# Kernel tuning notes

Measured on AMD Instinct MI355X. Metric: run time of the kernel, lower is better.

The kernel has to match this reference:

```python
import jax, jax.numpy as jnp
import numpy as np

NUM_TYPES = 4  # unique atom types, e.g. H,C,N,O
N_DESC = 384   # descriptor width (nDescriptors())


def setup_inputs() -> dict:
    key = jax.random.key(0)
    k1, k2, k3 = jax.random.split(key, 3)
    n_confs, n_atoms = 2048, 64
    coords = jax.random.normal(k1, (n_confs, n_atoms, 3), dtype=jnp.float32)
    atom_types = jax.random.randint(k2, (n_confs, n_atoms), 0, NUM_TYPES, dtype=jnp.int64)
    W = jax.random.normal(k3, (3, N_DESC), dtype=jnp.float32)
    return {"coords": coords, "atom_types": atom_types, "W": W}


def reference(coords, atom_types, W):
    n_confs, n_atoms, _ = coords.shape
    # stub descriptor computer: per-atom descriptor, (n_confs*n_atoms, N_DESC)
    desc = jnp.tanh(coords.reshape(-1, 3) @ W)
    at2type = atom_types.reshape(-1)                      # (N,)
    # conformer index for every atom: [0,0,...,0,1,1,...]
    at2conf = jnp.repeat(jnp.arange(n_confs, dtype=jnp.int64), n_atoms)
    # stable sort by atom type (routing permutation)
    perm = jnp.argsort(at2type, stable=True)              # (N,)
    desc_sorted = desc[perm]                              # gather (N, N_DESC)
    at2conf_sorted = at2conf[perm]                        # (N,)
    at_type_count = jnp.bincount(at2type, length=NUM_TYPES)  # split sizes per type
    # per-type buckets = desc_sorted split at cumsum(at_type_count); returned
    # concatenated with counts to keep shapes static under jit.
    return desc_sorted, at2conf_sorted, at_type_count
```

## Files before the change

kernel.cpp:

```cpp
#include <hip/hip_runtime.h>

#define NDESC 384
#define NTYPES 4
#define ATOMS_PER_CONF 64
#define BLOCK_ATOMS 128

typedef unsigned int uint32;
typedef unsigned long long u64;

__device__ __forceinline__ float fast_tanh(float x) {
  float e = __builtin_amdgcn_exp2f(x * 2.8853900817779268f);
  return 1.0f - 2.0f * __builtin_amdgcn_rcpf(1.0f + e);
}

__global__ __launch_bounds__(BLOCK_ATOMS) void hist_kernel(
    const int* __restrict__ types, uint32* __restrict__ blockHist, int n) {
  __shared__ uint32 cnt[NTYPES];
  int tid = threadIdx.x;
  if (tid < NTYPES) cnt[tid] = 0;
  __syncthreads();
  int idx = blockIdx.x * BLOCK_ATOMS + tid;
  int ty = (idx < n) ? types[idx] : -1;
  int lane = tid & 63;
  for (int t = 0; t < NTYPES; ++t) {
    u64 m = __ballot(ty == t);
    if (lane == 0) atomicAdd(&cnt[t], (uint32)__popcll(m));
  }
  __syncthreads();
  if (tid < NTYPES) blockHist[blockIdx.x * NTYPES + tid] = cnt[tid];
}

__global__ __launch_bounds__(256) void scan_kernel(
    const uint32* __restrict__ blockHist, uint32* __restrict__ blockOff,
    float* __restrict__ outCounts, int nb) {
  __shared__ uint32 totals[NTYPES];
  int tid = threadIdx.x;
  int wave = tid >> 6;
  int lane = tid & 63;

  uint32 sum = 0;
  for (int b = lane; b < nb; b += 64) sum += blockHist[b * NTYPES + wave];
  for (int off = 32; off > 0; off >>= 1) sum += __shfl_down(sum, off);
  if (lane == 0) totals[wave] = sum;
  __syncthreads();

  uint32 base = 0;
  for (int t = 0; t < wave; ++t) base += totals[t];

  uint32 carry = 0;
  for (int c = 0; c * 64 < nb; ++c) {
    int b = c * 64 + lane;
    uint32 v = (b < nb) ? blockHist[b * NTYPES + wave] : 0;
    uint32 orig = v;
    for (int off = 1; off < 64; off <<= 1) {
      uint32 nv = __shfl_up(v, off);
      if (lane >= off) v += nv;
    }
    if (b < nb) blockOff[b * NTYPES + wave] = base + carry + (v - orig);
    carry += __shfl(v, 63);
  }
  if (tid < NTYPES) outCounts[tid] = (float)totals[tid];
}

__global__ __launch_bounds__(384) void main_kernel(
    const float* __restrict__ coords, const int* __restrict__ types,
    const float* __restrict__ W, const uint32* __restrict__ blockOff,
    float* __restrict__ descOut, float* __restrict__ confOut, int n) {
  __shared__ float sW[3 * NDESC];
  __shared__ float sC[BLOCK_ATOMS][3];
  __shared__ uint32 sPos[BLOCK_ATOMS];
  __shared__ int sValid[BLOCK_ATOMS];
  __shared__ uint32 waveCnt[BLOCK_ATOMS / 64][NTYPES];

  int tid = threadIdx.x;
  int base = blockIdx.x * BLOCK_ATOMS;

  for (int i = tid; i < 3 * NDESC; i += 384) sW[i] = W[i];
  if (tid < BLOCK_ATOMS * 3) {
    int g = base * 3 + tid;
    sC[tid / 3][tid % 3] = (g < n * 3) ? coords[g] : 0.0f;
  }

  int idx = base + tid;
  int ty = -1;
  if (tid < BLOCK_ATOMS && idx < n) ty = types[idx];
  int wave = tid >> 6, lane = tid & 63;
  int myrank = 0;
  if (tid < BLOCK_ATOMS) {
    for (int t = 0; t < NTYPES; ++t) {
      u64 m = __ballot(ty == t);
      if (lane == 0) waveCnt[wave][t] = (uint32)__popcll(m);
      if (t == ty) myrank = (int)__popcll(m & ((1ull << lane) - 1ull));
    }
  }
  __syncthreads();
  if (tid < BLOCK_ATOMS) {
    if (ty >= 0) {
      for (int w = 0; w < wave; ++w) myrank += (int)waveCnt[w][ty];
      uint32 pos = blockOff[blockIdx.x * NTYPES + ty] + (uint32)myrank;
      sPos[tid] = pos;
      sValid[tid] = 1;
      confOut[pos] = (float)(idx >> 6);
    } else {
      sPos[tid] = 0;
      sValid[tid] = 0;
    }
  }
  __syncthreads();

  int r = tid / 96;
  int c = tid - r * 96;
  int d0 = 4 * c;
  float w00 = sW[d0], w01 = sW[d0 + 1], w02 = sW[d0 + 2], w03 = sW[d0 + 3];
  float w10 = sW[NDESC + d0], w11 = sW[NDESC + d0 + 1],
        w12 = sW[NDESC + d0 + 2], w13 = sW[NDESC + d0 + 3];
  float w20 = sW[2 * NDESC + d0], w21 = sW[2 * NDESC + d0 + 1],
        w22 = sW[2 * NDESC + d0 + 2], w23 = sW[2 * NDESC + d0 + 3];

  bool full = (base + BLOCK_ATOMS <= n);
  if (full) {
#pragma unroll 4
    for (int a0 = 0; a0 < BLOCK_ATOMS; a0 += 4) {
      int a = a0 + r;
      uint32 pos = sPos[a];
      float c0 = sC[a][0], c1 = sC[a][1], c2 = sC[a][2];
      float4 v;
      v.x = fast_tanh(c0 * w00 + c1 * w10 + c2 * w20);
      v.y = fast_tanh(c0 * w01 + c1 * w11 + c2 * w21);
      v.z = fast_tanh(c0 * w02 + c1 * w12 + c2 * w22);
      v.w = fast_tanh(c0 * w03 + c1 * w13 + c2 * w23);
      *reinterpret_cast<float4*>(descOut + pos * (uint32)NDESC + d0) = v;
    }
  } else {
    for (int a0 = 0; a0 < BLOCK_ATOMS; a0 += 4) {
      int a = a0 + r;
      uint32 pos = sPos[a];
      float c0 = sC[a][0], c1 = sC[a][1], c2 = sC[a][2];
      float4 v;
      v.x = fast_tanh(c0 * w00 + c1 * w10 + c2 * w20);
      v.y = fast_tanh(c0 * w01 + c1 * w11 + c2 * w21);
      v.z = fast_tanh(c0 * w02 + c1 * w12 + c2 * w22);
      v.w = fast_tanh(c0 * w03 + c1 * w13 + c2 * w23);
      if (sValid[a]) {
        *reinterpret_cast<float4*>(descOut + pos * (uint32)NDESC + d0) = v;
      }
    }
  }
}

extern "C" void kernel_launch(void* const* d_in, const int* in_sizes, int n_in,
                              void* d_out, int out_size, void* d_ws, size_t ws_size,
                              hipStream_t stream) {
  const float* coords = (const float*)d_in[0];
  const int* types = (const int*)d_in[1];
  const float* W = (const float*)d_in[2];

  int n = in_sizes[1];
  int nb = (n + BLOCK_ATOMS - 1) / BLOCK_ATOMS;

  uint32* blockHist = (uint32*)d_ws;
  uint32* blockOff = blockHist + (size_t)nb * NTYPES;

  float* descOut = (float*)d_out;
  float* confOut = descOut + (size_t)n * NDESC;
  float* countsOut = confOut + n;

  hipLaunchKernelGGL(hist_kernel, dim3(nb), dim3(BLOCK_ATOMS), 0, stream,
                     types, blockHist, n);
  hipLaunchKernelGGL(scan_kernel, dim3(1), dim3(256), 0, stream,
                     blockHist, blockOff, countsOut, nb);
  hipLaunchKernelGGL(main_kernel, dim3(nb), dim3(384), 0, stream,
                     coords, types, W, blockOff, descOut, confOut, n);
}
```

Measured before the change: 53.03 us.

## Fuse histogram, scan and scatter into one cooperative kernel with grid sync

Replaces the three-kernel pipeline (per-block type histogram, single-block scan, scatter/compute) with one cooperative kernel. Each block publishes its type histogram, waits at a grid-wide barrier, then computes its own prefix offsets and per-type totals by reducing the histogram array directly. Block size doubles to 256 atoms so the grid is small enough to be co-resident. This removes two kernel launches and the serial single-block scan. In exchange, every block has to be resident at once, and the barrier stalls all blocks until the slowest has finished its histogram.

```diff
diff --git a/kernel.cpp b/kernel.cpp
--- a/kernel.cpp
+++ b/kernel.cpp
@@ -1,84 +1,42 @@
 #include <hip/hip_runtime.h>
+#include <hip/hip_cooperative_groups.h>
 
 #define NDESC 384
 #define NTYPES 4
-#define ATOMS_PER_CONF 64
-#define BLOCK_ATOMS 128
+#define BLOCK_ATOMS 256
+#define NTHREADS 384
 
 typedef unsigned int uint32;
 typedef unsigned long long u64;
+
+namespace cg = cooperative_groups;
 
 __device__ __forceinline__ float fast_tanh(float x) {
   float e = __builtin_amdgcn_exp2f(x * 2.8853900817779268f);
   return 1.0f - 2.0f * __builtin_amdgcn_rcpf(1.0f + e);
 }
 
-__global__ __launch_bounds__(BLOCK_ATOMS) void hist_kernel(
-    const int* __restrict__ types, uint32* __restrict__ blockHist, int n) {
-  __shared__ uint32 cnt[NTYPES];
-  int tid = threadIdx.x;
-  if (tid < NTYPES) cnt[tid] = 0;
-  __syncthreads();
-  int idx = blockIdx.x * BLOCK_ATOMS + tid;
-  int ty = (idx < n) ? types[idx] : -1;
-  int lane = tid & 63;
-  for (int t = 0; t < NTYPES; ++t) {
-    u64 m = __ballot(ty == t);
-    if (lane == 0) atomicAdd(&cnt[t], (uint32)__popcll(m));
-  }
-  __syncthreads();
-  if (tid < NTYPES) blockHist[blockIdx.x * NTYPES + tid] = cnt[tid];
-}
-
-__global__ __launch_bounds__(256) void scan_kernel(
-    const uint32* __restrict__ blockHist, uint32* __restrict__ blockOff,
-    float* __restrict__ outCounts, int nb) {
-  __shared__ uint32 totals[NTYPES];
-  int tid = threadIdx.x;
-  int wave = tid >> 6;
-  int lane = tid & 63;
-
-  uint32 sum = 0;
-  for (int b = lane; b < nb; b += 64) sum += blockHist[b * NTYPES + wave];
-  for (int off = 32; off > 0; off >>= 1) sum += __shfl_down(sum, off);
-  if (lane == 0) totals[wave] = sum;
-  __syncthreads();
-
-  uint32 base = 0;
-  for (int t = 0; t < wave; ++t) base += totals[t];
-
-  uint32 carry = 0;
-  for (int c = 0; c * 64 < nb; ++c) {
-    int b = c * 64 + lane;
-    uint32 v = (b < nb) ? blockHist[b * NTYPES + wave] : 0;
-    uint32 orig = v;
-    for (int off = 1; off < 64; off <<= 1) {
-      uint32 nv = __shfl_up(v, off);
-      if (lane >= off) v += nv;
-    }
-    if (b < nb) blockOff[b * NTYPES + wave] = base + carry + (v - orig);
-    carry += __shfl(v, 63);
-  }
-  if (tid < NTYPES) outCounts[tid] = (float)totals[tid];
-}
-
-__global__ __launch_bounds__(384) void main_kernel(
+__global__ __launch_bounds__(NTHREADS, 3) void fused_kernel(
     const float* __restrict__ coords, const int* __restrict__ types,
-    const float* __restrict__ W, const uint32* __restrict__ blockOff,
-    float* __restrict__ descOut, float* __restrict__ confOut, int n) {
+    const float* __restrict__ W, uint32* __restrict__ blockHist,
+    float* __restrict__ descOut, float* __restrict__ confOut,
+    float* __restrict__ countsOut, int n, int nb) {
   __shared__ float sW[3 * NDESC];
   __shared__ float sC[BLOCK_ATOMS][3];
   __shared__ uint32 sPos[BLOCK_ATOMS];
   __shared__ int sValid[BLOCK_ATOMS];
   __shared__ uint32 waveCnt[BLOCK_ATOMS / 64][NTYPES];
+  __shared__ uint32 sTot[NTYPES];
+  __shared__ uint32 sOff[NTYPES];
 
   int tid = threadIdx.x;
-  int base = blockIdx.x * BLOCK_ATOMS;
+  int bid = blockIdx.x;
+  int base = bid * BLOCK_ATOMS;
 
-  for (int i = tid; i < 3 * NDESC; i += 384) sW[i] = W[i];
-  if (tid < BLOCK_ATOMS * 3) {
-    int g = base * 3 + tid;
-    sC[tid / 3][tid % 3] = (g < n * 3) ? coords[g] : 0.0f;
+  for (int i = tid; i < 3 * NDESC; i += NTHREADS) sW[i] = W[i];
+  for (int i = tid; i < BLOCK_ATOMS * 3; i += NTHREADS) {
+    int g = base * 3 + i;
+    sC[i / 3][i % 3] = (g < n * 3) ? coords[g] : 0.0f;
   }
 
   int idx = base + tid;
@@ -94,10 +52,43 @@
     }
   }
   __syncthreads();
+  if (tid < NTYPES) {
+    uint32 s = 0;
+    for (int w = 0; w < BLOCK_ATOMS / 64; ++w) s += waveCnt[w][tid];
+    blockHist[bid * NTYPES + tid] = s;
+  }
+  if (tid < BLOCK_ATOMS && ty >= 0) {
+    for (int w = 0; w < wave; ++w) myrank += (int)waveCnt[w][ty];
+  }
+
+  cg::this_grid().sync();
+
+  if (wave < NTYPES) {
+    int t = wave;
+    uint32 tot = 0, pre = 0;
+    for (int b = lane; b < nb; b += 64) {
+      uint32 h = blockHist[b * NTYPES + t];
+      tot += h;
+      if (b < bid) pre += h;
+    }
+    for (int off = 32; off > 0; off >>= 1) {
+      tot += __shfl_down(tot, off);
+      pre += __shfl_down(pre, off);
+    }
+    if (lane == 0) { sTot[t] = tot; sOff[t] = pre; }
+  }
+  __syncthreads();
+  if (tid < NTYPES) {
+    uint32 b = 0;
+    for (int t = 0; t < tid; ++t) b += sTot[t];
+    sOff[tid] += b;
+    if (bid == 0) countsOut[tid] = (float)sTot[tid];
+  }
+  __syncthreads();
+
   if (tid < BLOCK_ATOMS) {
     if (ty >= 0) {
-      for (int w = 0; w < wave; ++w) myrank += (int)waveCnt[w][ty];
-      uint32 pos = blockOff[blockIdx.x * NTYPES + ty] + (uint32)myrank;
+      uint32 pos = sOff[ty] + (uint32)myrank;
       sPos[tid] = pos;
       sValid[tid] = 1;
       confOut[pos] = (float)(idx >> 6);
@@ -129,7 +120,7 @@
       v.y = fast_tanh(c0 * w01 + c1 * w11 + c2 * w21);
       v.z = fast_tanh(c0 * w02 + c1 * w12 + c2 * w22);
       v.w = fast_tanh(c0 * w03 + c1 * w13 + c2 * w23);
-      *reinterpret_cast<float4*>(descOut + pos * (uint32)NDESC + d0) = v;
+      *reinterpret_cast<float4*>(descOut + (size_t)pos * NDESC + d0) = v;
     }
   } else {
     for (int a0 = 0; a0 < BLOCK_ATOMS; a0 += 4) {
@@ -142,7 +133,7 @@
       v.z = fast_tanh(c0 * w02 + c1 * w12 + c2 * w22);
       v.w = fast_tanh(c0 * w03 + c1 * w13 + c2 * w23);
       if (sValid[a]) {
-        *reinterpret_cast<float4*>(descOut + pos * (uint32)NDESC + d0) = v;
+        *reinterpret_cast<float4*>(descOut + (size_t)pos * NDESC + d0) = v;
       }
     }
   }
@@ -159,16 +150,14 @@
   int nb = (n + BLOCK_ATOMS - 1) / BLOCK_ATOMS;
 
   uint32* blockHist = (uint32*)d_ws;
-  uint32* blockOff = blockHist + (size_t)nb * NTYPES;
 
   float* descOut = (float*)d_out;
   float* confOut = descOut + (size_t)n * NDESC;
   float* countsOut = confOut + n;
 
-  hipLaunchKernelGGL(hist_kernel, dim3(nb), dim3(BLOCK_ATOMS), 0, stream,
-                     types, blockHist, n);
-  hipLaunchKernelGGL(scan_kernel, dim3(1), dim3(256), 0, stream,
-                     blockHist, blockOff, countsOut, nb);
-  hipLaunchKernelGGL(main_kernel, dim3(nb), dim3(384), 0, stream,
-                     coords, types, W, blockOff, descOut, confOut, n);
+  void* args[] = {(void*)&coords, (void*)&types, (void*)&W, (void*)&blockHist,
+                  (void*)&descOut, (void*)&confOut, (void*)&countsOut,
+                  (void*)&n, (void*)&nb};
+  hipLaunchCooperativeKernel((const void*)fused_kernel, dim3(nb), dim3(NTHREADS),
+                             args, 0, stream);
 }
```

After: 89.70 us. 69.1% more time.
